# Kernel tuning notes

Measured on AMD Instinct MI355X. Metric: run time of the kernel, lower is better.

Reference implementation:

```python
import jax, jax.numpy as jnp
import numpy as np

B = 16384
MOTION = 128      # motion_size
USED = 3          # used_motions
LAT = 32          # latent_size
H1 = 512
H2 = 512
MOE = 8
IN = MOTION * (USED - 1) + LAT  # 288 (used_angles = 0)


def setup_inputs() -> dict:
    key = jax.random.key(0)
    ks = jax.random.split(key, 14)
    s = 0.02
    return {
        "motions": jax.random.normal(ks[0], (B, MOTION * (USED - 1)), jnp.float32),
        "z": jax.random.normal(ks[1], (B, LAT), jnp.float32),
        # gate MLP params
        "gw1": jax.random.normal(ks[2], (IN, H1), jnp.float32) * s,
        "gb1": jnp.zeros((H1,), jnp.float32),
        "gw2": jax.random.normal(ks[3], (H1, H2), jnp.float32) * s,
        "gb2": jnp.zeros((H2,), jnp.float32),
        "gw3": jax.random.normal(ks[4], (H2, MOE), jnp.float32) * s,
        "gb3": jnp.zeros((MOE,), jnp.float32),
        # stacked expert params: layer k weight [MOE, in_k, out_k]
        "W1": jax.random.normal(ks[5], (MOE, IN, H1), jnp.float32) * s,
        "b1": jnp.zeros((MOE, H1), jnp.float32),
        "W2": jax.random.normal(ks[6], (MOE, H1 + LAT, H2), jnp.float32) * s,
        "b2": jnp.zeros((MOE, H2), jnp.float32),
        "W3": jax.random.normal(ks[7], (MOE, H2 + LAT, MOTION), jnp.float32) * s,
        "b3": jnp.zeros((MOE, MOTION), jnp.float32),
    }


def reference(motions, z, gw1, gb1, gw2, gb2, gw3, gb3, W1, b1, W2, b2, W3, b3):
    # used_angles == 0 -> angles is empty; input = concat([motions, z])
    x = jnp.concatenate([motions, z], axis=1)            # [B, IN]

    # gate: 3-layer ELU MLP -> per-expert blend weights [B, MOE]
    para = jax.nn.elu(x @ gw1 + gb1)
    para = jax.nn.elu(para @ gw2 + gb2)
    para = jax.nn.elu(para @ gw3 + gb3)

    # all experts batched via stacked weights (replaces Python loop)
    zb = jnp.broadcast_to(z[None], (MOE, B, LAT))        # z re-concatenated per layer
    h = jax.nn.elu(jnp.einsum('bi,eio->ebo', x, W1) + b1[:, None, :])              # [E,B,H1]
    h = jax.nn.elu(jnp.einsum('ebi,eio->ebo', jnp.concatenate([h, zb], -1), W2)
                   + b2[:, None, :])                                               # [E,B,H2]
    h = jax.nn.elu(jnp.einsum('ebi,eio->ebo', jnp.concatenate([h, zb], -1), W3)
                   + b3[:, None, :])                                               # [E,B,M]

    # gated combine, then divide by Frobenius norm of the whole gate matrix
    out = jnp.einsum('be,ebm->bm', para, h)              # [B, MOTION]
    out = out / jnp.linalg.norm(para)
    return jax.nn.sigmoid(out)
```

## Files before the change

### kernel.cpp

```cpp
#include <hip/hip_runtime.h>


typedef __attribute__((ext_vector_type(8))) short bf16x8;
typedef __attribute__((ext_vector_type(4))) float f32x4;
#define MFMA(a, b, c) __builtin_amdgcn_mfma_f32_16x16x32_bf16(a, b, c, 0, 0, 0)

#define STRIDE 552

__device__ __forceinline__ float elu_f(float x) { return x > 0.f ? x : (__expf(x) - 1.f); }

__device__ __forceinline__ ushort f2bf(float f) {
    union { float f; unsigned u; } v; v.f = f;
    unsigned r = v.u + 0x7fffu + ((v.u >> 16) & 1u);
    return (ushort)(r >> 16);
}
__device__ __forceinline__ float bf2f(ushort u) {
    union { unsigned u; float f; } v; v.u = ((unsigned)u) << 16;
    return v.f;
}

__global__ void prep_xz(const float* __restrict__ motions, const float* __restrict__ z,
                        ushort* __restrict__ xz) {
    int i = blockIdx.x * 256 + threadIdx.x;
    int r = i / 72, c = i % 72;
    float4 v = (c < 64) ? ((const float4*)motions)[r * 64 + c]
                        : ((const float4*)z)[r * 8 + (c - 64)];
    ushort4 o;
    o.x = f2bf(v.x); o.y = f2bf(v.y); o.z = f2bf(v.z); o.w = f2bf(v.w);
    *(ushort4*)(xz + (size_t)r * 288 + c * 4) = o;
}

__global__ void prep_transpose(const float* __restrict__ in, ushort* __restrict__ out,
                               int K, int N) {
    __shared__ float tile[32][33];
    const int e = blockIdx.z;
    const float* inp = in + (size_t)e * K * N;
    ushort* outp = out + (size_t)e * N * K;
    const int k0 = blockIdx.x * 32, n0 = blockIdx.y * 32;
    const int tx = threadIdx.x, ty = threadIdx.y;
    #pragma unroll
    for (int i = 0; i < 4; ++i)
        tile[ty + i * 8][tx] = inp[(size_t)(k0 + ty + i * 8) * N + n0 + tx];
    __syncthreads();
    #pragma unroll
    for (int i = 0; i < 4; ++i)
        outp[(size_t)(n0 + ty + i * 8) * K + k0 + tx] = f2bf(tile[tx][ty + i * 8]);
}

__global__ __launch_bounds__(512, 2) void gate_kernel(
    const ushort* __restrict__ xz,
    const ushort* __restrict__ gw1t, const float* __restrict__ gb1,
    const ushort* __restrict__ gw2t, const float* __restrict__ gb2,
    const float* __restrict__ gw3, const float* __restrict__ gb3,
    float* __restrict__ para, float* __restrict__ partial)
{
    __shared__ ushort hs[64 * STRIDE];
    __shared__ float red[512];
    const int t = threadIdx.x;
    const int lane = t & 63, w = t >> 6;
    const int lr = lane & 15, lk = lane >> 4;
    const int r0 = blockIdx.x * 64;
    const ushort* xrow = xz + (size_t)r0 * 288;
    const int n0 = w * 64;

    {
        f32x4 acc[4][4] = {};
        for (int ks = 0; ks < 9; ++ks) {
            bf16x8 a[4], b[4];
            #pragma unroll
            for (int mf = 0; mf < 4; ++mf)
                a[mf] = *(const bf16x8*)(xrow + (size_t)(mf * 16 + lr) * 288 + ks * 32 + lk * 8);
            #pragma unroll
            for (int nf = 0; nf < 4; ++nf)
                b[nf] = *(const bf16x8*)(gw1t + (size_t)(n0 + nf * 16 + lr) * 288 + ks * 32 + lk * 8);
            #pragma unroll
            for (int mf = 0; mf < 4; ++mf)
                #pragma unroll
                for (int nf = 0; nf < 4; ++nf)
                    acc[mf][nf] = MFMA(a[mf], b[nf], acc[mf][nf]);
        }
        #pragma unroll
        for (int nf = 0; nf < 4; ++nf) {
            int col = n0 + nf * 16 + lr;
            float bb = gb1[col];
            #pragma unroll
            for (int mf = 0; mf < 4; ++mf)
                #pragma unroll
                for (int j = 0; j < 4; ++j)
                    hs[(mf * 16 + lk * 4 + j) * STRIDE + col] = f2bf(elu_f(acc[mf][nf][j] + bb));
        }
    }
    __syncthreads();

    {
        f32x4 acc[4][4] = {};
        for (int ks = 0; ks < 16; ++ks) {
            bf16x8 a[4], b[4];
            #pragma unroll
            for (int mf = 0; mf < 4; ++mf)
                a[mf] = *(const bf16x8*)&hs[(mf * 16 + lr) * STRIDE + ks * 32 + lk * 8];
            #pragma unroll
            for (int nf = 0; nf < 4; ++nf)
                b[nf] = *(const bf16x8*)(gw2t + (size_t)(n0 + nf * 16 + lr) * 512 + ks * 32 + lk * 8);
            #pragma unroll
            for (int mf = 0; mf < 4; ++mf)
                #pragma unroll
                for (int nf = 0; nf < 4; ++nf)
                    acc[mf][nf] = MFMA(a[mf], b[nf], acc[mf][nf]);
        }
        __syncthreads();
        #pragma unroll
        for (int nf = 0; nf < 4; ++nf) {
            int col = n0 + nf * 16 + lr;
            float bb = gb2[col];
            #pragma unroll
            for (int mf = 0; mf < 4; ++mf)
                #pragma unroll
                for (int j = 0; j < 4; ++j)
                    hs[(mf * 16 + lk * 4 + j) * STRIDE + col] = f2bf(elu_f(acc[mf][nf][j] + bb));
        }
    }
    __syncthreads();

    {
        const int row = t >> 3, e = t & 7;
        float acc = 0.f;
        for (int k = 0; k < 512; k += 8) {
            uint4 hv = *(const uint4*)&hs[row * STRIDE + k];
            acc += bf2f((ushort)(hv.x)) * gw3[(k + 0) * 8 + e];
            acc += bf2f((ushort)(hv.x >> 16)) * gw3[(k + 1) * 8 + e];
            acc += bf2f((ushort)(hv.y)) * gw3[(k + 2) * 8 + e];
            acc += bf2f((ushort)(hv.y >> 16)) * gw3[(k + 3) * 8 + e];
            acc += bf2f((ushort)(hv.z)) * gw3[(k + 4) * 8 + e];
            acc += bf2f((ushort)(hv.z >> 16)) * gw3[(k + 5) * 8 + e];
            acc += bf2f((ushort)(hv.w)) * gw3[(k + 6) * 8 + e];
            acc += bf2f((ushort)(hv.w >> 16)) * gw3[(k + 7) * 8 + e];
        }
        float p = elu_f(acc + gb3[e]);
        para[(size_t)(r0 + row) * 8 + e] = p;
        red[t] = p * p;
    }
    __syncthreads();
    for (int s = 256; s >= 1; s >>= 1) {
        if (t < s) red[t] += red[t + s];
        __syncthreads();
    }
    if (t == 0) partial[blockIdx.x] = red[0];
}

__global__ void finalize_kernel(const float* __restrict__ partial, float* __restrict__ invn) {
    __shared__ float red[256];
    const int t = threadIdx.x;
    red[t] = partial[t];
    __syncthreads();
    for (int s = 128; s >= 1; s >>= 1) {
        if (t < s) red[t] += red[t + s];
        __syncthreads();
    }
    if (t == 0) invn[0] = 1.0f / sqrtf(red[0]);
}

__global__ __launch_bounds__(512, 2) void expert_kernel(
    const ushort* __restrict__ xz, const float* __restrict__ z,
    const ushort* __restrict__ W1t, const float* __restrict__ b1,
    const ushort* __restrict__ W2t, const float* __restrict__ b2,
    const ushort* __restrict__ W3t, const float* __restrict__ b3,
    const float* __restrict__ para, const float* __restrict__ invn,
    float* __restrict__ out)
{
    __shared__ ushort hs[64 * STRIDE];
    __shared__ float ps[64 * 8];
    const int t = threadIdx.x;
    const int lane = t & 63, w = t >> 6;
    const int lr = lane & 15, lk = lane >> 4;
    const int r0 = blockIdx.x * 64;
    const ushort* xrow = xz + (size_t)r0 * 288;
    const int n0 = w * 64;

    for (int i = t; i < 2048; i += 512) {
        int r = i >> 5, c = i & 31;
        hs[r * STRIDE + 512 + c] = f2bf(z[(size_t)(r0 + r) * 32 + c]);
    }
    ps[t] = para[(size_t)r0 * 8 + t];
    const float inv_norm = invn[0];

    float oacc[4][4];
    #pragma unroll
    for (int mf = 0; mf < 4; ++mf)
        #pragma unroll
        for (int j = 0; j < 4; ++j) oacc[mf][j] = 0.f;

    for (int e = 0; e < 8; ++e) {
        __syncthreads();

        {
            const ushort* Wt = W1t + (size_t)e * 512 * 288;
            f32x4 acc[4][4] = {};
            for (int ks = 0; ks < 9; ++ks) {
                bf16x8 a[4], b[4];
                #pragma unroll
                for (int mf = 0; mf < 4; ++mf)
                    a[mf] = *(const bf16x8*)(xrow + (size_t)(mf * 16 + lr) * 288 + ks * 32 + lk * 8);
                #pragma unroll
                for (int nf = 0; nf < 4; ++nf)
                    b[nf] = *(const bf16x8*)(Wt + (size_t)(n0 + nf * 16 + lr) * 288 + ks * 32 + lk * 8);
                #pragma unroll
                for (int mf = 0; mf < 4; ++mf)
                    #pragma unroll
                    for (int nf = 0; nf < 4; ++nf)
                        acc[mf][nf] = MFMA(a[mf], b[nf], acc[mf][nf]);
            }
            #pragma unroll
            for (int nf = 0; nf < 4; ++nf) {
                int col = n0 + nf * 16 + lr;
                float bb = b1[e * 512 + col];
                #pragma unroll
                for (int mf = 0; mf < 4; ++mf)
                    #pragma unroll
                    for (int j = 0; j < 4; ++j)
                        hs[(mf * 16 + lk * 4 + j) * STRIDE + col] = f2bf(elu_f(acc[mf][nf][j] + bb));
            }
        }
        __syncthreads();

        {
            const ushort* Wt = W2t + (size_t)e * 512 * 544;
            f32x4 acc[4][4] = {};
            for (int ks = 0; ks < 17; ++ks) {
                bf16x8 a[4], b[4];
                #pragma unroll
                for (int mf = 0; mf < 4; ++mf)
                    a[mf] = *(const bf16x8*)&hs[(mf * 16 + lr) * STRIDE + ks * 32 + lk * 8];
                #pragma unroll
                for (int nf = 0; nf < 4; ++nf)
                    b[nf] = *(const bf16x8*)(Wt + (size_t)(n0 + nf * 16 + lr) * 544 + ks * 32 + lk * 8);
                #pragma unroll
                for (int mf = 0; mf < 4; ++mf)
                    #pragma unroll
                    for (int nf = 0; nf < 4; ++nf)
                        acc[mf][nf] = MFMA(a[mf], b[nf], acc[mf][nf]);
            }
            __syncthreads();
            #pragma unroll
            for (int nf = 0; nf < 4; ++nf) {
                int col = n0 + nf * 16 + lr;
                float bb = b2[e * 512 + col];
                #pragma unroll
                for (int mf = 0; mf < 4; ++mf)
                    #pragma unroll
                    for (int j = 0; j < 4; ++j)
                        hs[(mf * 16 + lk * 4 + j) * STRIDE + col] = f2bf(elu_f(acc[mf][nf][j] + bb));
            }
        }
        __syncthreads();

        {
            const ushort* Wt = W3t + (size_t)e * 128 * 544;
            f32x4 acc3[4] = {};
            const int c0 = w * 16;
            for (int ks = 0; ks < 17; ++ks) {
                bf16x8 b = *(const bf16x8*)(Wt + (size_t)(c0 + lr) * 544 + ks * 32 + lk * 8);
                #pragma unroll
                for (int mf = 0; mf < 4; ++mf) {
                    bf16x8 a = *(const bf16x8*)&hs[(mf * 16 + lr) * STRIDE + ks * 32 + lk * 8];
                    acc3[mf] = MFMA(a, b, acc3[mf]);
                }
            }
            float bb = b3[e * 128 + c0 + lr];
            #pragma unroll
            for (int mf = 0; mf < 4; ++mf)
                #pragma unroll
                for (int j = 0; j < 4; ++j) {
                    int row = mf * 16 + lk * 4 + j;
                    float h3 = elu_f(acc3[mf][j] + bb);
                    oacc[mf][j] += ps[row * 8 + e] * h3;
                }
        }
    }

    #pragma unroll
    for (int mf = 0; mf < 4; ++mf)
        #pragma unroll
        for (int j = 0; j < 4; ++j) {
            int row = mf * 16 + lk * 4 + j;
            float v = oacc[mf][j] * inv_norm;
            out[(size_t)(r0 + row) * 128 + w * 16 + lr] = 1.0f / (1.0f + __expf(-v));
        }
}

extern "C" void kernel_launch(void* const* d_in, const int* in_sizes, int n_in,
                              void* d_out, int out_size, void* d_ws, size_t ws_size,
                              hipStream_t stream) {
    const float* motions = (const float*)d_in[0];
    const float* z   = (const float*)d_in[1];
    const float* gw1 = (const float*)d_in[2];
    const float* gb1 = (const float*)d_in[3];
    const float* gw2 = (const float*)d_in[4];
    const float* gb2 = (const float*)d_in[5];
    const float* gw3 = (const float*)d_in[6];
    const float* gb3 = (const float*)d_in[7];
    const float* W1  = (const float*)d_in[8];
    const float* b1  = (const float*)d_in[9];
    const float* W2  = (const float*)d_in[10];
    const float* b2  = (const float*)d_in[11];
    const float* W3  = (const float*)d_in[12];
    const float* b3  = (const float*)d_in[13];
    float* out = (float*)d_out;

    char* W = (char*)d_ws;
    ushort* xz      = (ushort*)(W);
    ushort* gw1t    = (ushort*)(W + 9437184);
    ushort* gw2t    = (ushort*)(W + 9732096);
    ushort* W1t     = (ushort*)(W + 10256384);
    ushort* W2t     = (ushort*)(W + 12615680);
    ushort* W3t     = (ushort*)(W + 17072128);
    float*  para    = (float*) (W + 18186240);
    float*  partial = (float*) (W + 18710528);
    float*  invn    = (float*) (W + 18711552);

    prep_xz<<<dim3(4608), dim3(256), 0, stream>>>(motions, z, xz);
    prep_transpose<<<dim3(9, 16, 1), dim3(32, 8), 0, stream>>>(gw1, gw1t, 288, 512);
    prep_transpose<<<dim3(16, 16, 1), dim3(32, 8), 0, stream>>>(gw2, gw2t, 512, 512);
    prep_transpose<<<dim3(9, 16, 8), dim3(32, 8), 0, stream>>>(W1, W1t, 288, 512);
    prep_transpose<<<dim3(17, 16, 8), dim3(32, 8), 0, stream>>>(W2, W2t, 544, 512);
    prep_transpose<<<dim3(17, 4, 8), dim3(32, 8), 0, stream>>>(W3, W3t, 544, 128);

    gate_kernel<<<dim3(256), dim3(512), 0, stream>>>(xz, gw1t, gb1, gw2t, gb2, gw3, gb3,
                                                     para, partial);
    finalize_kernel<<<dim3(1), dim3(256), 0, stream>>>(partial, invn);
    expert_kernel<<<dim3(256), dim3(512), 0, stream>>>(xz, z, W1t, b1, W2t, b2, W3t, b3,
                                                       para, invn, out);
}
```

Measured before the change: 324.4 us.

## Double waves per block, prefetch weight fragments, and stage expert inputs in LDS

```diff
diff --git a/kernel.cpp b/kernel.cpp
--- a/kernel.cpp
+++ b/kernel.cpp
@@ -6,6 +6,7 @@
 #define MFMA(a, b, c) __builtin_amdgcn_mfma_f32_16x16x32_bf16(a, b, c, 0, 0, 0)
 
 #define STRIDE 552
+#define XSTRIDE 296
 
 __device__ __forceinline__ float elu_f(float x) { return x > 0.f ? x : (__expf(x) - 1.f); }
 
@@ -18,6 +19,7 @@
     union { unsigned u; float f; } v; v.u = ((unsigned)u) << 16;
     return v.f;
 }
+__device__ __forceinline__ bf16x8 ldg8(const ushort* p) { return *(const bf16x8*)p; }
 
 __global__ void prep_xz(const float* __restrict__ motions, const float* __restrict__ z,
                         ushort* __restrict__ xz) {
@@ -47,7 +49,7 @@
         outp[(size_t)(n0 + ty + i * 8) * K + k0 + tx] = f2bf(tile[tx][ty + i * 8]);
 }
 
-__global__ __launch_bounds__(512, 2) void gate_kernel(
+__global__ __launch_bounds__(1024, 1) void gate_kernel(
     const ushort* __restrict__ xz,
     const ushort* __restrict__ gw1t, const float* __restrict__ gb1,
     const ushort* __restrict__ gw2t, const float* __restrict__ gb2,
@@ -61,26 +63,29 @@
     const int lr = lane & 15, lk = lane >> 4;
     const int r0 = blockIdx.x * 64;
     const ushort* xrow = xz + (size_t)r0 * 288;
-    const int n0 = w * 64;
+    const int n0 = w * 32;
 
     {
-        f32x4 acc[4][4] = {};
+        const ushort* B0 = gw1t + (size_t)(n0 + lr) * 288 + lk * 8;
+        const ushort* B1 = gw1t + (size_t)(n0 + 16 + lr) * 288 + lk * 8;
+        f32x4 acc[4][2] = {};
+        bf16x8 bc0 = ldg8(B0), bc1 = ldg8(B1);
         for (int ks = 0; ks < 9; ++ks) {
-            bf16x8 a[4], b[4];
+            bf16x8 bn0 = bc0, bn1 = bc1;
+            if (ks < 8) { bn0 = ldg8(B0 + (ks + 1) * 32); bn1 = ldg8(B1 + (ks + 1) * 32); }
+            bf16x8 a[4];
             #pragma unroll
             for (int mf = 0; mf < 4; ++mf)
-                a[mf] = *(const bf16x8*)(xrow + (size_t)(mf * 16 + lr) * 288 + ks * 32 + lk * 8);
-            #pragma unroll
-            for (int nf = 0; nf < 4; ++nf)
-                b[nf] = *(const bf16x8*)(gw1t + (size_t)(n0 + nf * 16 + lr) * 288 + ks * 32 + lk * 8);
-            #pragma unroll
-            for (int mf = 0; mf < 4; ++mf)
-                #pragma unroll
-                for (int nf = 0; nf < 4; ++nf)
-                    acc[mf][nf] = MFMA(a[mf], b[nf], acc[mf][nf]);
+                a[mf] = ldg8(xrow + (size_t)(mf * 16 + lr) * 288 + ks * 32 + lk * 8);
+            #pragma unroll
+            for (int mf = 0; mf < 4; ++mf) {
+                acc[mf][0] = MFMA(a[mf], bc0, acc[mf][0]);
+                acc[mf][1] = MFMA(a[mf], bc1, acc[mf][1]);
+            }
+            bc0 = bn0; bc1 = bn1;
         }
         #pragma unroll
-        for (int nf = 0; nf < 4; ++nf) {
+        for (int nf = 0; nf < 2; ++nf) {
             int col = n0 + nf * 16 + lr;
             float bb = gb1[col];
             #pragma unroll
@@ -93,24 +98,27 @@
     __syncthreads();
 
     {
-        f32x4 acc[4][4] = {};
+        const ushort* B0 = gw2t + (size_t)(n0 + lr) * 512 + lk * 8;
+        const ushort* B1 = gw2t + (size_t)(n0 + 16 + lr) * 512 + lk * 8;
+        f32x4 acc[4][2] = {};
+        bf16x8 bc0 = ldg8(B0), bc1 = ldg8(B1);
         for (int ks = 0; ks < 16; ++ks) {
-            bf16x8 a[4], b[4];
+            bf16x8 bn0 = bc0, bn1 = bc1;
+            if (ks < 15) { bn0 = ldg8(B0 + (ks + 1) * 32); bn1 = ldg8(B1 + (ks + 1) * 32); }
+            bf16x8 a[4];
             #pragma unroll
             for (int mf = 0; mf < 4; ++mf)
                 a[mf] = *(const bf16x8*)&hs[(mf * 16 + lr) * STRIDE + ks * 32 + lk * 8];
             #pragma unroll
-            for (int nf = 0; nf < 4; ++nf)
-                b[nf] = *(const bf16x8*)(gw2t + (size_t)(n0 + nf * 16 + lr) * 512 + ks * 32 + lk * 8);
-            #pragma unroll
-            for (int mf = 0; mf < 4; ++mf)
-                #pragma unroll
-                for (int nf = 0; nf < 4; ++nf)
-                    acc[mf][nf] = MFMA(a[mf], b[nf], acc[mf][nf]);
+            for (int mf = 0; mf < 4; ++mf) {
+                acc[mf][0] = MFMA(a[mf], bc0, acc[mf][0]);
+                acc[mf][1] = MFMA(a[mf], bc1, acc[mf][1]);
+            }
+            bc0 = bn0; bc1 = bn1;
         }
         __syncthreads();
         #pragma unroll
-        for (int nf = 0; nf < 4; ++nf) {
+        for (int nf = 0; nf < 2; ++nf) {
             int col = n0 + nf * 16 + lr;
             float bb = gb2[col];
             #pragma unroll
@@ -122,7 +130,7 @@
     }
     __syncthreads();
 
-    {
+    if (t < 512) {
         const int row = t >> 3, e = t & 7;
         float acc = 0.f;
         for (int k = 0; k < 512; k += 8) {
@@ -160,7 +168,7 @@
     if (t == 0) invn[0] = 1.0f / sqrtf(red[0]);
 }
 
-__global__ __launch_bounds__(512, 2) void expert_kernel(
+__global__ __launch_bounds__(1024, 1) void expert_kernel(
     const ushort* __restrict__ xz, const float* __restrict__ z,
     const ushort* __restrict__ W1t, const float* __restrict__ b1,
     const ushort* __restrict__ W2t, const float* __restrict__ b2,
@@ -169,49 +177,54 @@
     float* __restrict__ out)
 {
     __shared__ ushort hs[64 * STRIDE];
+    __shared__ ushort xs[64 * XSTRIDE];
     __shared__ float ps[64 * 8];
     const int t = threadIdx.x;
     const int lane = t & 63, w = t >> 6;
     const int lr = lane & 15, lk = lane >> 4;
     const int r0 = blockIdx.x * 64;
-    const ushort* xrow = xz + (size_t)r0 * 288;
-    const int n0 = w * 64;
-
-    for (int i = t; i < 2048; i += 512) {
+    const int n0 = w * 32;
+    const int rb = (w >> 2) * 16;
+    const int c0 = (w & 3) * 32;
+
+    for (int i = t; i < 2304; i += 1024) {
+        int r = i / 36, c = i % 36;
+        *(uint4*)&xs[r * XSTRIDE + c * 8] = *(const uint4*)(xz + (size_t)(r0 + r) * 288 + c * 8);
+    }
+    for (int i = t; i < 2048; i += 1024) {
         int r = i >> 5, c = i & 31;
         hs[r * STRIDE + 512 + c] = f2bf(z[(size_t)(r0 + r) * 32 + c]);
     }
-    ps[t] = para[(size_t)r0 * 8 + t];
+    if (t < 512) ps[t] = para[(size_t)r0 * 8 + t];
     const float inv_norm = invn[0];
 
-    float oacc[4][4];
-    #pragma unroll
-    for (int mf = 0; mf < 4; ++mf)
-        #pragma unroll
-        for (int j = 0; j < 4; ++j) oacc[mf][j] = 0.f;
+    f32x4 oacc[2] = {};
 
     for (int e = 0; e < 8; ++e) {
         __syncthreads();
 
         {
             const ushort* Wt = W1t + (size_t)e * 512 * 288;
-            f32x4 acc[4][4] = {};
+            const ushort* B0 = Wt + (size_t)(n0 + lr) * 288 + lk * 8;
+            const ushort* B1 = Wt + (size_t)(n0 + 16 + lr) * 288 + lk * 8;
+            f32x4 acc[4][2] = {};
+            bf16x8 bc0 = ldg8(B0), bc1 = ldg8(B1);
             for (int ks = 0; ks < 9; ++ks) {
-                bf16x8 a[4], b[4];
+                bf16x8 bn0 = bc0, bn1 = bc1;
+                if (ks < 8) { bn0 = ldg8(B0 + (ks + 1) * 32); bn1 = ldg8(B1 + (ks + 1) * 32); }
+                bf16x8 a[4];
                 #pragma unroll
                 for (int mf = 0; mf < 4; ++mf)
-                    a[mf] = *(const bf16x8*)(xrow + (size_t)(mf * 16 + lr) * 288 + ks * 32 + lk * 8);
-                #pragma unroll
-                for (int nf = 0; nf < 4; ++nf)
-                    b[nf] = *(const bf16x8*)(Wt + (size_t)(n0 + nf * 16 + lr) * 288 + ks * 32 + lk * 8);
-                #pragma unroll
-                for (int mf = 0; mf < 4; ++mf)
-                    #pragma unroll
-                    for (int nf = 0; nf < 4; ++nf)
-                        acc[mf][nf] = MFMA(a[mf], b[nf], acc[mf][nf]);
-            }
-            #pragma unroll
-            for (int nf = 0; nf < 4; ++nf) {
+                    a[mf] = *(const bf16x8*)&xs[(mf * 16 + lr) * XSTRIDE + ks * 32 + lk * 8];
+                #pragma unroll
+                for (int mf = 0; mf < 4; ++mf) {
+                    acc[mf][0] = MFMA(a[mf], bc0, acc[mf][0]);
+                    acc[mf][1] = MFMA(a[mf], bc1, acc[mf][1]);
+                }
+                bc0 = bn0; bc1 = bn1;
+            }
+            #pragma unroll
+            for (int nf = 0; nf < 2; ++nf) {
                 int col = n0 + nf * 16 + lr;
                 float bb = b1[e * 512 + col];
                 #pragma unroll
@@ -225,24 +238,27 @@
 
         {
             const ushort* Wt = W2t + (size_t)e * 512 * 544;
-            f32x4 acc[4][4] = {};
+            const ushort* B0 = Wt + (size_t)(n0 + lr) * 544 + lk * 8;
+            const ushort* B1 = Wt + (size_t)(n0 + 16 + lr) * 544 + lk * 8;
+            f32x4 acc[4][2] = {};
+            bf16x8 bc0 = ldg8(B0), bc1 = ldg8(B1);
             for (int ks = 0; ks < 17; ++ks) {
-                bf16x8 a[4], b[4];
+                bf16x8 bn0 = bc0, bn1 = bc1;
+                if (ks < 16) { bn0 = ldg8(B0 + (ks + 1) * 32); bn1 = ldg8(B1 + (ks + 1) * 32); }
+                bf16x8 a[4];
                 #pragma unroll
                 for (int mf = 0; mf < 4; ++mf)
                     a[mf] = *(const bf16x8*)&hs[(mf * 16 + lr) * STRIDE + ks * 32 + lk * 8];
                 #pragma unroll
-                for (int nf = 0; nf < 4; ++nf)
-                    b[nf] = *(const bf16x8*)(Wt + (size_t)(n0 + nf * 16 + lr) * 544 + ks * 32 + lk * 8);
-                #pragma unroll
-                for (int mf = 0; mf < 4; ++mf)
-                    #pragma unroll
-                    for (int nf = 0; nf < 4; ++nf)
-                        acc[mf][nf] = MFMA(a[mf], b[nf], acc[mf][nf]);
+                for (int mf = 0; mf < 4; ++mf) {
+                    acc[mf][0] = MFMA(a[mf], bc0, acc[mf][0]);
+                    acc[mf][1] = MFMA(a[mf], bc1, acc[mf][1]);
+                }
+                bc0 = bn0; bc1 = bn1;
             }
             __syncthreads();
             #pragma unroll
-            for (int nf = 0; nf < 4; ++nf) {
+            for (int nf = 0; nf < 2; ++nf) {
                 int col = n0 + nf * 16 + lr;
                 float bb = b2[e * 512 + col];
                 #pragma unroll
@@ -256,35 +272,38 @@
 
         {
             const ushort* Wt = W3t + (size_t)e * 128 * 544;
-            f32x4 acc3[4] = {};
-            const int c0 = w * 16;
+            const ushort* B0 = Wt + (size_t)(c0 + lr) * 544 + lk * 8;
+            const ushort* B1 = Wt + (size_t)(c0 + 16 + lr) * 544 + lk * 8;
+            f32x4 acc3[2] = {};
+            bf16x8 bc0 = ldg8(B0), bc1 = ldg8(B1);
             for (int ks = 0; ks < 17; ++ks) {
-                bf16x8 b = *(const bf16x8*)(Wt + (size_t)(c0 + lr) * 544 + ks * 32 + lk * 8);
-                #pragma unroll
-                for (int mf = 0; mf < 4; ++mf) {
-                    bf16x8 a = *(const bf16x8*)&hs[(mf * 16 + lr) * STRIDE + ks * 32 + lk * 8];
-                    acc3[mf] = MFMA(a, b, acc3[mf]);
+                bf16x8 bn0 = bc0, bn1 = bc1;
+                if (ks < 16) { bn0 = ldg8(B0 + (ks + 1) * 32); bn1 = ldg8(B1 + (ks + 1) * 32); }
+                bf16x8 a = *(const bf16x8*)&hs[(rb + lr) * STRIDE + ks * 32 + lk * 8];
+                acc3[0] = MFMA(a, bc0, acc3[0]);
+                acc3[1] = MFMA(a, bc1, acc3[1]);
+                bc0 = bn0; bc1 = bn1;
+            }
+            #pragma unroll
+            for (int nf = 0; nf < 2; ++nf) {
+                float bb = b3[e * 128 + c0 + nf * 16 + lr];
+                #pragma unroll
+                for (int j = 0; j < 4; ++j) {
+                    int row = rb + lk * 4 + j;
+                    float h3 = elu_f(acc3[nf][j] + bb);
+                    oacc[nf][j] += ps[row * 8 + e] * h3;
                 }
             }
-            float bb = b3[e * 128 + c0 + lr];
-            #pragma unroll
-            for (int mf = 0; mf < 4; ++mf)
-                #pragma unroll
-                for (int j = 0; j < 4; ++j) {
-                    int row = mf * 16 + lk * 4 + j;
-                    float h3 = elu_f(acc3[mf][j] + bb);
-                    oacc[mf][j] += ps[row * 8 + e] * h3;
-                }
         }
     }
 
     #pragma unroll
-    for (int mf = 0; mf < 4; ++mf)
+    for (int nf = 0; nf < 2; ++nf)
         #pragma unroll
         for (int j = 0; j < 4; ++j) {
-            int row = mf * 16 + lk * 4 + j;
-            float v = oacc[mf][j] * inv_norm;
-            out[(size_t)(r0 + row) * 128 + w * 16 + lr] = 1.0f / (1.0f + __expf(-v));
+            int row = rb + lk * 4 + j;
+            float v = oacc[nf][j] * inv_norm;
+            out[(size_t)(r0 + row) * 128 + c0 + nf * 16 + lr] = 1.0f / (1.0f + __expf(-v));
         }
 }
 
@@ -325,9 +344,9 @@
     prep_transpose<<<dim3(17, 16, 8), dim3(32, 8), 0, stream>>>(W2, W2t, 544, 512);
     prep_transpose<<<dim3(17, 4, 8), dim3(32, 8), 0, stream>>>(W3, W3t, 544, 128);
 
-    gate_kernel<<<dim3(256), dim3(512), 0, stream>>>(xz, gw1t, gb1, gw2t, gb2, gw3, gb3,
-                                                     para, partial);
+    gate_kernel<<<dim3(256), dim3(1024), 0, stream>>>(xz, gw1t, gb1, gw2t, gb2, gw3, gb3,
+                                                      para, partial);
     finalize_kernel<<<dim3(1), dim3(256), 0, stream>>>(partial, invn);
-    expert_kernel<<<dim3(256), dim3(512), 0, stream>>>(xz, z, W1t, b1, W2t, b2, W3t, b3,
-                                                       para, invn, out);
-}
+    expert_kernel<<<dim3(256), dim3(1024), 0, stream>>>(xz, z, W1t, b1, W2t, b2, W3t, b3,
+                                                        para, invn, out);
+}
```

Measured after the change: 283.7 us. 1.14x faster.

## Use 1024-thread blocks with row-split waves, prefetched weights and vectorized epilogues

Applied to the files above, without the earlier changes.

```diff
diff --git a/kernel.cpp b/kernel.cpp
--- a/kernel.cpp
+++ b/kernel.cpp
@@ -6,6 +6,7 @@
 #define MFMA(a, b, c) __builtin_amdgcn_mfma_f32_16x16x32_bf16(a, b, c, 0, 0, 0)
 
 #define STRIDE 552
+#define XSTRIDE 296
 
 __device__ __forceinline__ float elu_f(float x) { return x > 0.f ? x : (__expf(x) - 1.f); }
 
@@ -18,6 +19,7 @@
     union { unsigned u; float f; } v; v.u = ((unsigned)u) << 16;
     return v.f;
 }
+__device__ __forceinline__ bf16x8 ldg8(const ushort* p) { return *(const bf16x8*)p; }
 
 __global__ void prep_xz(const float* __restrict__ motions, const float* __restrict__ z,
                         ushort* __restrict__ xz) {
@@ -47,7 +49,7 @@
         outp[(size_t)(n0 + ty + i * 8) * K + k0 + tx] = f2bf(tile[tx][ty + i * 8]);
 }
 
-__global__ __launch_bounds__(512, 2) void gate_kernel(
+__global__ __launch_bounds__(1024, 1) void gate_kernel(
     const ushort* __restrict__ xz,
     const ushort* __restrict__ gw1t, const float* __restrict__ gb1,
     const ushort* __restrict__ gw2t, const float* __restrict__ gb2,
@@ -61,68 +63,95 @@
     const int lr = lane & 15, lk = lane >> 4;
     const int r0 = blockIdx.x * 64;
     const ushort* xrow = xz + (size_t)r0 * 288;
-    const int n0 = w * 64;
+    const int mg = w >> 3;
+    const int n0 = (w & 7) * 64;
 
     {
-        f32x4 acc[4][4] = {};
+        f32x4 acc[2][4] = {};
+        bf16x8 bc[4], bn[4];
+        #pragma unroll
+        for (int nf = 0; nf < 4; ++nf)
+            bc[nf] = ldg8(gw1t + (size_t)(n0 + nf * 16 + lr) * 288 + lk * 8);
         for (int ks = 0; ks < 9; ++ks) {
-            bf16x8 a[4], b[4];
-            #pragma unroll
-            for (int mf = 0; mf < 4; ++mf)
-                a[mf] = *(const bf16x8*)(xrow + (size_t)(mf * 16 + lr) * 288 + ks * 32 + lk * 8);
-            #pragma unroll
-            for (int nf = 0; nf < 4; ++nf)
-                b[nf] = *(const bf16x8*)(gw1t + (size_t)(n0 + nf * 16 + lr) * 288 + ks * 32 + lk * 8);
-            #pragma unroll
-            for (int mf = 0; mf < 4; ++mf)
+            if (ks < 8) {
                 #pragma unroll
                 for (int nf = 0; nf < 4; ++nf)
-                    acc[mf][nf] = MFMA(a[mf], b[nf], acc[mf][nf]);
+                    bn[nf] = ldg8(gw1t + (size_t)(n0 + nf * 16 + lr) * 288 + (ks + 1) * 32 + lk * 8);
+            }
+            bf16x8 a[2];
+            #pragma unroll
+            for (int mf = 0; mf < 2; ++mf)
+                a[mf] = ldg8(xrow + (size_t)(mg * 32 + mf * 16 + lr) * 288 + ks * 32 + lk * 8);
+            #pragma unroll
+            for (int mf = 0; mf < 2; ++mf)
+                #pragma unroll
+                for (int nf = 0; nf < 4; ++nf)
+                    acc[mf][nf] = MFMA(bc[nf], a[mf], acc[mf][nf]);
+            #pragma unroll
+            for (int nf = 0; nf < 4; ++nf) bc[nf] = bn[nf];
         }
         #pragma unroll
         for (int nf = 0; nf < 4; ++nf) {
-            int col = n0 + nf * 16 + lr;
-            float bb = gb1[col];
-            #pragma unroll
-            for (int mf = 0; mf < 4; ++mf)
-                #pragma unroll
-                for (int j = 0; j < 4; ++j)
-                    hs[(mf * 16 + lk * 4 + j) * STRIDE + col] = f2bf(elu_f(acc[mf][nf][j] + bb));
+            const int nb = n0 + nf * 16 + lk * 4;
+            const float4 bb = *(const float4*)&gb1[nb];
+            #pragma unroll
+            for (int mf = 0; mf < 2; ++mf) {
+                const int row = mg * 32 + mf * 16 + lr;
+                ushort4 o;
+                o.x = f2bf(elu_f(acc[mf][nf][0] + bb.x));
+                o.y = f2bf(elu_f(acc[mf][nf][1] + bb.y));
+                o.z = f2bf(elu_f(acc[mf][nf][2] + bb.z));
+                o.w = f2bf(elu_f(acc[mf][nf][3] + bb.w));
+                *(ushort4*)&hs[row * STRIDE + nb] = o;
+            }
         }
     }
     __syncthreads();
 
     {
-        f32x4 acc[4][4] = {};
+        f32x4 acc[2][4] = {};
+        bf16x8 bc[4], bn[4];
+        #pragma unroll
+        for (int nf = 0; nf < 4; ++nf)
+            bc[nf] = ldg8(gw2t + (size_t)(n0 + nf * 16 + lr) * 512 + lk * 8);
         for (int ks = 0; ks < 16; ++ks) {
-            bf16x8 a[4], b[4];
-            #pragma unroll
-            for (int mf = 0; mf < 4; ++mf)
-                a[mf] = *(const bf16x8*)&hs[(mf * 16 + lr) * STRIDE + ks * 32 + lk * 8];
-            #pragma unroll
-            for (int nf = 0; nf < 4; ++nf)
-                b[nf] = *(const bf16x8*)(gw2t + (size_t)(n0 + nf * 16 + lr) * 512 + ks * 32 + lk * 8);
-            #pragma unroll
-            for (int mf = 0; mf < 4; ++mf)
+            if (ks < 15) {
                 #pragma unroll
                 for (int nf = 0; nf < 4; ++nf)
-                    acc[mf][nf] = MFMA(a[mf], b[nf], acc[mf][nf]);
+                    bn[nf] = ldg8(gw2t + (size_t)(n0 + nf * 16 + lr) * 512 + (ks + 1) * 32 + lk * 8);
+            }
+            bf16x8 a[2];
+            #pragma unroll
+            for (int mf = 0; mf < 2; ++mf)
+                a[mf] = *(const bf16x8*)&hs[(mg * 32 + mf * 16 + lr) * STRIDE + ks * 32 + lk * 8];
+            #pragma unroll
+            for (int mf = 0; mf < 2; ++mf)
+                #pragma unroll
+                for (int nf = 0; nf < 4; ++nf)
+                    acc[mf][nf] = MFMA(bc[nf], a[mf], acc[mf][nf]);
+            #pragma unroll
+            for (int nf = 0; nf < 4; ++nf) bc[nf] = bn[nf];
         }
         __syncthreads();
         #pragma unroll
         for (int nf = 0; nf < 4; ++nf) {
-            int col = n0 + nf * 16 + lr;
-            float bb = gb2[col];
-            #pragma unroll
-            for (int mf = 0; mf < 4; ++mf)
-                #pragma unroll
-                for (int j = 0; j < 4; ++j)
-                    hs[(mf * 16 + lk * 4 + j) * STRIDE + col] = f2bf(elu_f(acc[mf][nf][j] + bb));
-        }
-    }
-    __syncthreads();
-
-    {
+            const int nb = n0 + nf * 16 + lk * 4;
+            const float4 bb = *(const float4*)&gb2[nb];
+            #pragma unroll
+            for (int mf = 0; mf < 2; ++mf) {
+                const int row = mg * 32 + mf * 16 + lr;
+                ushort4 o;
+                o.x = f2bf(elu_f(acc[mf][nf][0] + bb.x));
+                o.y = f2bf(elu_f(acc[mf][nf][1] + bb.y));
+                o.z = f2bf(elu_f(acc[mf][nf][2] + bb.z));
+                o.w = f2bf(elu_f(acc[mf][nf][3] + bb.w));
+                *(ushort4*)&hs[row * STRIDE + nb] = o;
+            }
+        }
+    }
+    __syncthreads();
+
+    if (t < 512) {
         const int row = t >> 3, e = t & 7;
         float acc = 0.f;
         for (int k = 0; k < 512; k += 8) {
@@ -160,7 +189,7 @@
     if (t == 0) invn[0] = 1.0f / sqrtf(red[0]);
 }
 
-__global__ __launch_bounds__(512, 2) void expert_kernel(
+__global__ __launch_bounds__(1024, 1) void expert_kernel(
     const ushort* __restrict__ xz, const float* __restrict__ z,
     const ushort* __restrict__ W1t, const float* __restrict__ b1,
     const ushort* __restrict__ W2t, const float* __restrict__ b2,
@@ -169,123 +198,159 @@
     float* __restrict__ out)
 {
     __shared__ ushort hs[64 * STRIDE];
+    __shared__ ushort xs[64 * XSTRIDE];
     __shared__ float ps[64 * 8];
     const int t = threadIdx.x;
     const int lane = t & 63, w = t >> 6;
     const int lr = lane & 15, lk = lane >> 4;
     const int r0 = blockIdx.x * 64;
-    const ushort* xrow = xz + (size_t)r0 * 288;
-    const int n0 = w * 64;
-
-    for (int i = t; i < 2048; i += 512) {
+    const int mg = w >> 3;
+    const int n0 = (w & 7) * 64;
+    const int rb = (w >> 2) * 16;
+    const int c0 = (w & 3) * 32;
+
+    for (int i = t; i < 2304; i += 1024) {
+        int r = i / 36, c = i % 36;
+        *(uint4*)&xs[r * XSTRIDE + c * 8] = *(const uint4*)(xz + (size_t)(r0 + r) * 288 + c * 8);
+    }
+    for (int i = t; i < 2048; i += 1024) {
         int r = i >> 5, c = i & 31;
         hs[r * STRIDE + 512 + c] = f2bf(z[(size_t)(r0 + r) * 32 + c]);
     }
-    ps[t] = para[(size_t)r0 * 8 + t];
+    if (t < 512) ps[t] = para[(size_t)r0 * 8 + t];
     const float inv_norm = invn[0];
 
-    float oacc[4][4];
-    #pragma unroll
-    for (int mf = 0; mf < 4; ++mf)
-        #pragma unroll
-        for (int j = 0; j < 4; ++j) oacc[mf][j] = 0.f;
+    f32x4 oacc[2] = {};
 
     for (int e = 0; e < 8; ++e) {
         __syncthreads();
 
         {
             const ushort* Wt = W1t + (size_t)e * 512 * 288;
-            f32x4 acc[4][4] = {};
+            f32x4 acc[2][4] = {};
+            bf16x8 bc[4], bn[4];
+            #pragma unroll
+            for (int nf = 0; nf < 4; ++nf)
+                bc[nf] = ldg8(Wt + (size_t)(n0 + nf * 16 + lr) * 288 + lk * 8);
             for (int ks = 0; ks < 9; ++ks) {
-                bf16x8 a[4], b[4];
-                #pragma unroll
-                for (int mf = 0; mf < 4; ++mf)
-                    a[mf] = *(const bf16x8*)(xrow + (size_t)(mf * 16 + lr) * 288 + ks * 32 + lk * 8);
-                #pragma unroll
-                for (int nf = 0; nf < 4; ++nf)
-                    b[nf] = *(const bf16x8*)(Wt + (size_t)(n0 + nf * 16 + lr) * 288 + ks * 32 + lk * 8);
-                #pragma unroll
-                for (int mf = 0; mf < 4; ++mf)
+                if (ks < 8) {
                     #pragma unroll
                     for (int nf = 0; nf < 4; ++nf)
-                        acc[mf][nf] = MFMA(a[mf], b[nf], acc[mf][nf]);
+                        bn[nf] = ldg8(Wt + (size_t)(n0 + nf * 16 + lr) * 288 + (ks + 1) * 32 + lk * 8);
+                }
+                bf16x8 a[2];
+                #pragma unroll
+                for (int mf = 0; mf < 2; ++mf)
+                    a[mf] = *(const bf16x8*)&xs[(mg * 32 + mf * 16 + lr) * XSTRIDE + ks * 32 + lk * 8];
+                #pragma unroll
+                for (int mf = 0; mf < 2; ++mf)
+                    #pragma unroll
+                    for (int nf = 0; nf < 4; ++nf)
+                        acc[mf][nf] = MFMA(bc[nf], a[mf], acc[mf][nf]);
+                #pragma unroll
+                for (int nf = 0; nf < 4; ++nf) bc[nf] = bn[nf];
             }
             #pragma unroll
             for (int nf = 0; nf < 4; ++nf) {
-                int col = n0 + nf * 16 + lr;
-                float bb = b1[e * 512 + col];
-                #pragma unroll
-                for (int mf = 0; mf < 4; ++mf)
-                    #pragma unroll
-                    for (int j = 0; j < 4; ++j)
-                        hs[(mf * 16 + lk * 4 + j) * STRIDE + col] = f2bf(elu_f(acc[mf][nf][j] + bb));
+                const int nb = n0 + nf * 16 + lk * 4;
+                const float4 bb = *(const float4*)&b1[e * 512 + nb];
+                #pragma unroll
+                for (int mf = 0; mf < 2; ++mf) {
+                    const int row = mg * 32 + mf * 16 + lr;
+                    ushort4 o;
+                    o.x = f2bf(elu_f(acc[mf][nf][0] + bb.x));
+                    o.y = f2bf(elu_f(acc[mf][nf][1] + bb.y));
+                    o.z = f2bf(elu_f(acc[mf][nf][2] + bb.z));
+                    o.w = f2bf(elu_f(acc[mf][nf][3] + bb.w));
+                    *(ushort4*)&hs[row * STRIDE + nb] = o;
+                }
             }
         }
         __syncthreads();
 
         {
             const ushort* Wt = W2t + (size_t)e * 512 * 544;
-            f32x4 acc[4][4] = {};
+            f32x4 acc[2][4] = {};
+            bf16x8 bc[4], bn[4];
+            #pragma unroll
+            for (int nf = 0; nf < 4; ++nf)
+                bc[nf] = ldg8(Wt + (size_t)(n0 + nf * 16 + lr) * 544 + lk * 8);
             for (int ks = 0; ks < 17; ++ks) {
-                bf16x8 a[4], b[4];
-                #pragma unroll
-                for (int mf = 0; mf < 4; ++mf)
-                    a[mf] = *(const bf16x8*)&hs[(mf * 16 + lr) * STRIDE + ks * 32 + lk * 8];
-                #pragma unroll
-                for (int nf = 0; nf < 4; ++nf)
-                    b[nf] = *(const bf16x8*)(Wt + (size_t)(n0 + nf * 16 + lr) * 544 + ks * 32 + lk * 8);
-                #pragma unroll
-                for (int mf = 0; mf < 4; ++mf)
+                if (ks < 16) {
                     #pragma unroll
                     for (int nf = 0; nf < 4; ++nf)
-                        acc[mf][nf] = MFMA(a[mf], b[nf], acc[mf][nf]);
+                        bn[nf] = ldg8(Wt + (size_t)(n0 + nf * 16 + lr) * 544 + (ks + 1) * 32 + lk * 8);
+                }
+                bf16x8 a[2];
+                #pragma unroll
+                for (int mf = 0; mf < 2; ++mf)
+                    a[mf] = *(const bf16x8*)&hs[(mg * 32 + mf * 16 + lr) * STRIDE + ks * 32 + lk * 8];
+                #pragma unroll
+                for (int mf = 0; mf < 2; ++mf)
+                    #pragma unroll
+                    for (int nf = 0; nf < 4; ++nf)
+                        acc[mf][nf] = MFMA(bc[nf], a[mf], acc[mf][nf]);
+                #pragma unroll
+                for (int nf = 0; nf < 4; ++nf) bc[nf] = bn[nf];
             }
             __syncthreads();
             #pragma unroll
             for (int nf = 0; nf < 4; ++nf) {
-                int col = n0 + nf * 16 + lr;
-                float bb = b2[e * 512 + col];
-                #pragma unroll
-                for (int mf = 0; mf < 4; ++mf)
-                    #pragma unroll
-                    for (int j = 0; j < 4; ++j)
-                        hs[(mf * 16 + lk * 4 + j) * STRIDE + col] = f2bf(elu_f(acc[mf][nf][j] + bb));
+                const int nb = n0 + nf * 16 + lk * 4;
+                const float4 bb = *(const float4*)&b2[e * 512 + nb];
+                #pragma unroll
+                for (int mf = 0; mf < 2; ++mf) {
+                    const int row = mg * 32 + mf * 16 + lr;
+                    ushort4 o;
+                    o.x = f2bf(elu_f(acc[mf][nf][0] + bb.x));
+                    o.y = f2bf(elu_f(acc[mf][nf][1] + bb.y));
+                    o.z = f2bf(elu_f(acc[mf][nf][2] + bb.z));
+                    o.w = f2bf(elu_f(acc[mf][nf][3] + bb.w));
+                    *(ushort4*)&hs[row * STRIDE + nb] = o;
+                }
             }
         }
         __syncthreads();
 
         {
             const ushort* Wt = W3t + (size_t)e * 128 * 544;
-            f32x4 acc3[4] = {};
-            const int c0 = w * 16;
+            f32x4 acc3[2] = {};
+            bf16x8 bc[2], bn[2];
+            #pragma unroll
+            for (int nf = 0; nf < 2; ++nf)
+                bc[nf] = ldg8(Wt + (size_t)(c0 + nf * 16 + lr) * 544 + lk * 8);
             for (int ks = 0; ks < 17; ++ks) {
-                bf16x8 b = *(const bf16x8*)(Wt + (size_t)(c0 + lr) * 544 + ks * 32 + lk * 8);
-                #pragma unroll
-                for (int mf = 0; mf < 4; ++mf) {
-                    bf16x8 a = *(const bf16x8*)&hs[(mf * 16 + lr) * STRIDE + ks * 32 + lk * 8];
-                    acc3[mf] = MFMA(a, b, acc3[mf]);
-                }
-            }
-            float bb = b3[e * 128 + c0 + lr];
-            #pragma unroll
-            for (int mf = 0; mf < 4; ++mf)
-                #pragma unroll
-                for (int j = 0; j < 4; ++j) {
-                    int row = mf * 16 + lk * 4 + j;
-                    float h3 = elu_f(acc3[mf][j] + bb);
-                    oacc[mf][j] += ps[row * 8 + e] * h3;
-                }
+                if (ks < 16) {
+                    #pragma unroll
+                    for (int nf = 0; nf < 2; ++nf)
+                        bn[nf] = ldg8(Wt + (size_t)(c0 + nf * 16 + lr) * 544 + (ks + 1) * 32 + lk * 8);
+                }
+                bf16x8 a = *(const bf16x8*)&hs[(rb + lr) * STRIDE + ks * 32 + lk * 8];
+                acc3[0] = MFMA(bc[0], a, acc3[0]);
+                acc3[1] = MFMA(bc[1], a, acc3[1]);
+                bc[0] = bn[0]; bc[1] = bn[1];
+            }
+            const float pse = ps[(rb + lr) * 8 + e];
+            #pragma unroll
+            for (int nf = 0; nf < 2; ++nf) {
+                const float4 bb = *(const float4*)&b3[e * 128 + c0 + nf * 16 + lk * 4];
+                oacc[nf][0] += pse * elu_f(acc3[nf][0] + bb.x);
+                oacc[nf][1] += pse * elu_f(acc3[nf][1] + bb.y);
+                oacc[nf][2] += pse * elu_f(acc3[nf][2] + bb.z);
+                oacc[nf][3] += pse * elu_f(acc3[nf][3] + bb.w);
+            }
         }
     }
 
     #pragma unroll
-    for (int mf = 0; mf < 4; ++mf)
-        #pragma unroll
-        for (int j = 0; j < 4; ++j) {
-            int row = mf * 16 + lk * 4 + j;
-            float v = oacc[mf][j] * inv_norm;
-            out[(size_t)(r0 + row) * 128 + w * 16 + lr] = 1.0f / (1.0f + __expf(-v));
-        }
+    for (int nf = 0; nf < 2; ++nf) {
+        float4 o;
+        o.x = 1.0f / (1.0f + __expf(-oacc[nf][0] * inv_norm));
+        o.y = 1.0f / (1.0f + __expf(-oacc[nf][1] * inv_norm));
+        o.z = 1.0f / (1.0f + __expf(-oacc[nf][2] * inv_norm));
+        o.w = 1.0f / (1.0f + __expf(-oacc[nf][3] * inv_norm));
+        *(float4*)&out[(size_t)(r0 + rb + lr) * 128 + c0 + nf * 16 + lk * 4] = o;
+    }
 }
 
 extern "C" void kernel_launch(void* const* d_in, const int* in_sizes, int n_in,
@@ -325,9 +390,9 @@
     prep_transpose<<<dim3(17, 16, 8), dim3(32, 8), 0, stream>>>(W2, W2t, 544, 512);
     prep_transpose<<<dim3(17, 4, 8), dim3(32, 8), 0, stream>>>(W3, W3t, 544, 128);
 
-    gate_kernel<<<dim3(256), dim3(512), 0, stream>>>(xz, gw1t, gb1, gw2t, gb2, gw3, gb3,
-                                                     para, partial);
+    gate_kernel<<<dim3(256), dim3(1024), 0, stream>>>(xz, gw1t, gb1, gw2t, gb2, gw3, gb3,
+                                                      para, partial);
     finalize_kernel<<<dim3(1), dim3(256), 0, stream>>>(partial, invn);
-    expert_kernel<<<dim3(256), dim3(512), 0, stream>>>(xz, z, W1t, b1, W2t, b2, W3t, b3,
-                                                       para, invn, out);
-}
+    expert_kernel<<<dim3(256), dim3(1024), 0, stream>>>(xz, z, W1t, b1, W2t, b2, W3t, b3,
+                                                        para, invn, out);
+}
```

After: 387.3 us. 1.19x slower.
